# Kernel optimization log

Measured on AMD Instinct MI355X. Metric: run time of the kernel, lower is better.

## Reference

```python
import jax, jax.numpy as jnp
import numpy as np
from jax import lax

D = 768; H = 8; DQ = D // H; NL = 6; FF = 3072; MAXREL = 100; NOUT = 1024
B = 8; T = 4096; CIN = 8
EPS = 1e-5
NREL = 2 * MAXREL - 1  # 199 learned relative positions, rel in [-99, 99]


def conv1d(x, w, b, stride=1, pad=1):
    # x [B,C,T], w [O,I,K]
    y = lax.conv_general_dilated(x, w, (stride,), [(pad, pad)],
                                 dimension_numbers=('NCH', 'OIH', 'NCH'))
    return y + b[None, :, None]


def bnorm(x, p):
    # eval-mode BatchNorm1d; p [4,C] = (gamma, beta, running_mean, running_var)
    g, be, m, v = p[0], p[1], p[2], p[3]
    return g[None, :, None] * (x - m[None, :, None]) * lax.rsqrt(v[None, :, None] + EPS) + be[None, :, None]


def resblock(x, c1w, c1b, b1, c2w, c2b, b2, rw, rb, br):
    h = jax.nn.relu(bnorm(conv1d(x, c1w, c1b, stride=2), b1))
    h = bnorm(conv1d(h, c2w, c2b), b2)
    res = bnorm(conv1d(x, rw, rb, stride=2, pad=0), br)
    return jax.nn.relu(h + res)


def layer_norm(x, g, b):
    mu = jnp.mean(x, axis=-1, keepdims=True)
    var = jnp.mean(jnp.square(x - mu), axis=-1, keepdims=True)
    return g * (x - mu) * lax.rsqrt(var + EPS) + b


def attention(x, wq, wk, wv, wo, rel):
    # x [B,L,D]; wq/wk/wv [H,D,DQ]; wo [H,DQ,D]; rel [H,NREL,DQ]
    L = x.shape[1]
    q = jnp.einsum('bld,hdk->bhlk', x, wq)
    k = jnp.einsum('bld,hdk->bhlk', x, wk)
    v = jnp.einsum('bld,hdk->bhlk', x, wv)
    logits = jnp.einsum('bhqk,bhmk->bhqm', q, k) / np.float32(np.sqrt(DQ))
    # relative positional logits: pos[b,h,i,j] = q[b,h,i] . rel[h, (j-i)+99] if |j-i|<100 else -1e8
    rel_logits = jnp.einsum('bhlk,hmk->bhlm', q, rel)  # [B,H,L,NREL]
    pos_idx = jnp.arange(L)[None, :] - jnp.arange(L)[:, None] + (MAXREL - 1)  # j - i + 99
    valid = (pos_idx >= 0) & (pos_idx < NREL)
    idxc = jnp.clip(pos_idx, 0, NREL - 1)
    pos = jnp.take_along_axis(rel_logits, idxc[None, None, :, :], axis=3)  # [B,H,L,L]
    logits = logits + jnp.where(valid[None, None], pos, jnp.float32(-1e8))
    probs = jax.nn.softmax(logits, axis=-1)
    o = jnp.einsum('bhqm,bhmk->bhqk', probs, v)
    return jnp.einsum('bhlk,hkd->bld', o, wo)


def forward(x_raw, rb1_c1w, rb1_c1b, rb1_bn1, rb1_c2w, rb1_c2b, rb1_bn2, rb1_rw, rb1_rb, rb1_bnr,
            rb23_c1w, rb23_c1b, rb23_bn1, rb23_c2w, rb23_c2b, rb23_bn2, rb23_rw, rb23_rb, rb23_bnr,
            w_in_w, w_in_b, wq, wk, wv, wo, rel_emb, ln1_g, ln1_b, ln2_g, ln2_b,
            ff1_w, ff1_b, ff2_w, ff2_b, w_out_w, w_out_b):
    x = jnp.transpose(x_raw, (0, 2, 1))  # [B, 8, T]
    x = resblock(x, rb1_c1w, rb1_c1b, rb1_bn1, rb1_c2w, rb1_c2b, rb1_bn2, rb1_rw, rb1_rb, rb1_bnr)
    for i in range(2):
        x = resblock(x, rb23_c1w[i], rb23_c1b[i], rb23_bn1[i], rb23_c2w[i], rb23_c2b[i],
                     rb23_bn2[i], rb23_rw[i], rb23_rb[i], rb23_bnr[i])
    x = jnp.transpose(x, (0, 2, 1))  # [B, L=T/8, D]
    x = x @ w_in_w.T + w_in_b
    for l in range(NL):  # post-norm transformer encoder layers
        x = layer_norm(x + attention(x, wq[l], wk[l], wv[l], wo[l], rel_emb[l]), ln1_g[l], ln1_b[l])
        h = jax.nn.relu(x @ ff1_w[l].T + ff1_b[l]) @ ff2_w[l].T + ff2_b[l]
        x = layer_norm(x + h, ln2_g[l], ln2_b[l])
    return x @ w_out_w.T + w_out_b


def setup_inputs() -> dict:
    key = jax.random.key(0)
    ks = iter(jax.random.split(key, 128))

    def w(shape, scale):
        return jax.random.normal(next(ks), shape, dtype=jnp.float32) * scale

    def bnp(*lead):
        g = 1.0 + 0.1 * jax.random.normal(next(ks), (*lead, D), dtype=jnp.float32)
        be = 0.1 * jax.random.normal(next(ks), (*lead, D), dtype=jnp.float32)
        m = 0.1 * jax.random.normal(next(ks), (*lead, D), dtype=jnp.float32)
        v = jax.random.uniform(next(ks), (*lead, D), minval=0.5, maxval=1.5, dtype=jnp.float32)
        return jnp.stack([g, be, m, v], axis=-2)  # [..., 4, D]

    inp = {}
    inp['x_raw'] = jax.random.normal(next(ks), (B, T, CIN), dtype=jnp.float32)
    inp['rb1_c1w'] = w((D, CIN, 3), 0.2); inp['rb1_c1b'] = w((D,), 0.02); inp['rb1_bn1'] = bnp()
    inp['rb1_c2w'] = w((D, D, 3), 0.02); inp['rb1_c2b'] = w((D,), 0.02); inp['rb1_bn2'] = bnp()
    inp['rb1_rw'] = w((D, CIN, 1), 0.2); inp['rb1_rb'] = w((D,), 0.02); inp['rb1_bnr'] = bnp()
    inp['rb23_c1w'] = w((2, D, D, 3), 0.02); inp['rb23_c1b'] = w((2, D), 0.02); inp['rb23_bn1'] = bnp(2)
    inp['rb23_c2w'] = w((2, D, D, 3), 0.02); inp['rb23_c2b'] = w((2, D), 0.02); inp['rb23_bn2'] = bnp(2)
    inp['rb23_rw'] = w((2, D, D, 1), 0.02); inp['rb23_rb'] = w((2, D), 0.02); inp['rb23_bnr'] = bnp(2)
    inp['w_in_w'] = w((D, D), 0.02); inp['w_in_b'] = w((D,), 0.02)
    sd = D ** -0.5
    inp['wq'] = w((NL, H, D, DQ), sd); inp['wk'] = w((NL, H, D, DQ), sd)
    inp['wv'] = w((NL, H, D, DQ), sd); inp['wo'] = w((NL, H, DQ, D), sd)
    inp['rel_emb'] = w((NL, H, NREL, DQ), DQ ** -0.5)
    inp['ln1_g'] = jnp.ones((NL, D), jnp.float32); inp['ln1_b'] = jnp.zeros((NL, D), jnp.float32)
    inp['ln2_g'] = jnp.ones((NL, D), jnp.float32); inp['ln2_b'] = jnp.zeros((NL, D), jnp.float32)
    inp['ff1_w'] = w((NL, FF, D), 0.02); inp['ff1_b'] = w((NL, FF), 0.02)
    inp['ff2_w'] = w((NL, D, FF), 0.02); inp['ff2_b'] = w((NL, D), 0.02)
    inp['w_out_w'] = w((NOUT, D), 0.02); inp['w_out_b'] = w((NOUT,), 0.02)
    return inp


def reference(x_raw, rb1_c1w, rb1_c1b, rb1_bn1, rb1_c2w, rb1_c2b, rb1_bn2, rb1_rw, rb1_rb, rb1_bnr,
              rb23_c1w, rb23_c1b, rb23_bn1, rb23_c2w, rb23_c2b, rb23_bn2, rb23_rw, rb23_rb, rb23_bnr,
              w_in_w, w_in_b, wq, wk, wv, wo, rel_emb, ln1_g, ln1_b, ln2_g, ln2_b,
              ff1_w, ff1_b, ff2_w, ff2_b, w_out_w, w_out_b):
    return forward(x_raw, rb1_c1w, rb1_c1b, rb1_bn1, rb1_c2w, rb1_c2b, rb1_bn2, rb1_rw, rb1_rb, rb1_bnr,
                   rb23_c1w, rb23_c1b, rb23_bn1, rb23_c2w, rb23_c2b, rb23_bn2, rb23_rw, rb23_rb, rb23_bnr,
                   w_in_w, w_in_b, wq, wk, wv, wo, rel_emb, ln1_g, ln1_b, ln2_g, ln2_b,
                   ff1_w, ff1_b, ff2_w, ff2_b, w_out_w, w_out_b)
```

## Files before the change

kernel.cpp:

```cpp
#include <hip/hip_runtime.h>
#include <math.h>

typedef __bf16 bf16;
typedef bf16 bf16x8 __attribute__((ext_vector_type(8)));
typedef bf16 bf16x4 __attribute__((ext_vector_type(4)));
typedef float f32x4 __attribute__((ext_vector_type(4)));
#define EPSF 1e-5f

__device__ __forceinline__ void ldg_lds16(const bf16* g, bf16* l) {
    __builtin_amdgcn_global_load_lds((const __attribute__((address_space(1))) void*)g,
                                     (__attribute__((address_space(3))) void*)l, 16, 0, 0);
}

template<bool BIAS, bool RESF, bool RELU, bool WF, bool WB>
__global__ __launch_bounds__(256) void mgemm_k(
    const bf16* __restrict__ A, const bf16* __restrict__ B,
    const float* __restrict__ bias, const float* __restrict__ resf,
    float* __restrict__ Cf, bf16* __restrict__ Cb,
    int K, int lda, int ldb, int ldc, int Nstore,
    int Z2, long long sA1, long long sA2, long long sB1, long long sB2,
    long long sC1, long long sC2)
{
    int z = blockIdx.z;
    int z1 = z / Z2, z2 = z - z1 * Z2;
    A += z1 * sA1 + z2 * sA2;
    B += z1 * sB1 + z2 * sB2;
    long long coff = z1 * sC1 + z2 * sC2;

    __shared__ __align__(16) bf16 As[4096];
    __shared__ __align__(16) bf16 Bs[4096];
    int tid = threadIdx.x, wid = tid >> 6, lane = tid & 63;
    int m0 = blockIdx.y * 128, n0 = blockIdx.x * 128;
    int wr = wid >> 1, wc = wid & 1;
    int lrow = lane & 15, lk8 = (lane >> 4) * 8;
    int srow = wid * 32 + (lane >> 2);
    int scol = (lane & 3) * 8;
    f32x4 acc[4][4] = {};

    for (int kt = 0; kt < K; kt += 32) {
        ldg_lds16(A + (size_t)(m0 + srow) * lda + kt + scol, As + wid * 1024);
        ldg_lds16(A + (size_t)(m0 + srow + 16) * lda + kt + scol, As + wid * 1024 + 512);
        ldg_lds16(B + (size_t)(n0 + srow) * ldb + kt + scol, Bs + wid * 1024);
        ldg_lds16(B + (size_t)(n0 + srow + 16) * ldb + kt + scol, Bs + wid * 1024 + 512);
        __syncthreads();
        bf16x8 af[4], bfr[4];
#pragma unroll
        for (int i = 0; i < 4; i++) {
            af[i]  = *(const bf16x8*)(As + (wr * 64 + i * 16 + lrow) * 32 + lk8);
            bfr[i] = *(const bf16x8*)(Bs + (wc * 64 + i * 16 + lrow) * 32 + lk8);
        }
#pragma unroll
        for (int i = 0; i < 4; i++)
#pragma unroll
            for (int j = 0; j < 4; j++)
                acc[i][j] = __builtin_amdgcn_mfma_f32_16x16x32_bf16(af[i], bfr[j], acc[i][j], 0, 0, 0);
        __syncthreads();
    }
    int mtop = m0 + wr * 64 + (lane >> 4) * 4;
    int ntop = n0 + wc * 64 + lrow;
#pragma unroll
    for (int mi = 0; mi < 4; mi++) {
#pragma unroll
        for (int r = 0; r < 4; r++) {
            int m = mtop + mi * 16 + r;
            long long ro = coff + (long long)m * ldc;
#pragma unroll
            for (int ni = 0; ni < 4; ni++) {
                int n = ntop + ni * 16;
                float v = acc[mi][ni][r];
                if (BIAS) v += bias[n];
                if (RESF) v += resf[ro + n];
                if (RELU) v = fmaxf(v, 0.f);
                if (n < Nstore) {
                    if (WF) Cf[ro + n] = v;
                    if (WB) Cb[ro + n] = (bf16)v;
                }
            }
        }
    }
}

template<bool RES, bool RELU>
__global__ __launch_bounds__(256) void conv_k(
    const bf16* __restrict__ in, const bf16* __restrict__ w,
    const float* __restrict__ scsh, const bf16* __restrict__ res, bf16* __restrict__ out,
    int KK, int stride, int rowoff, long long instrideB, long long outstrideB, int outoff,
    long long resstrideB)
{
    int z = blockIdx.z;
    int n0 = blockIdx.x * 128, m0 = blockIdx.y * 128;
    __shared__ __align__(16) bf16 As[4096];
    __shared__ __align__(16) bf16 Bs[4096];
    int tid = threadIdx.x, wid = tid >> 6, lane = tid & 63;
    int wr = wid >> 1, wc = wid & 1;
    int lrow = lane & 15, lk8 = (lane >> 4) * 8;
    int srow = wid * 32 + (lane >> 2);
    int scol = (lane & 3) * 8;
    const bf16* inz = in + (size_t)z * instrideB;
    f32x4 acc[4][4] = {};

    for (int kt = 0; kt < KK; kt += 32) {
        int kq = kt / 768;
        int ic0 = kt - kq * 768;
        ldg_lds16(inz + (size_t)((m0 + srow) * stride + kq + rowoff) * 768 + ic0 + scol, As + wid * 1024);
        ldg_lds16(inz + (size_t)((m0 + srow + 16) * stride + kq + rowoff) * 768 + ic0 + scol, As + wid * 1024 + 512);
        ldg_lds16(w + (size_t)(n0 + srow) * KK + kt + scol, Bs + wid * 1024);
        ldg_lds16(w + (size_t)(n0 + srow + 16) * KK + kt + scol, Bs + wid * 1024 + 512);
        __syncthreads();
        bf16x8 af[4], bfr[4];
#pragma unroll
        for (int i = 0; i < 4; i++) {
            af[i]  = *(const bf16x8*)(As + (wr * 64 + i * 16 + lrow) * 32 + lk8);
            bfr[i] = *(const bf16x8*)(Bs + (wc * 64 + i * 16 + lrow) * 32 + lk8);
        }
#pragma unroll
        for (int i = 0; i < 4; i++)
#pragma unroll
            for (int j = 0; j < 4; j++)
                acc[i][j] = __builtin_amdgcn_mfma_f32_16x16x32_bf16(af[i], bfr[j], acc[i][j], 0, 0, 0);
        __syncthreads();
    }
    bf16* outz = out + (size_t)z * outstrideB + (size_t)outoff * 768;
    const bf16* resz = res + (RES ? (size_t)z * resstrideB : 0);
    int mtop = m0 + wr * 64 + (lane >> 4) * 4;
    int ntop = n0 + wc * 64 + lrow;
#pragma unroll
    for (int mi = 0; mi < 4; mi++) {
#pragma unroll
        for (int r = 0; r < 4; r++) {
            int m = mtop + mi * 16 + r;
#pragma unroll
            for (int ni = 0; ni < 4; ni++) {
                int n = ntop + ni * 16;
                float v = acc[mi][ni][r] * scsh[n] + scsh[768 + n];
                if (RES) v += (float)resz[(size_t)m * 768 + n];
                if (RELU) v = fmaxf(v, 0.f);
                outz[(size_t)m * 768 + n] = (bf16)v;
            }
        }
    }
}

__global__ __launch_bounds__(256) void qkrel_k(
    const bf16* __restrict__ qkv, const float* __restrict__ relb, float* __restrict__ lg)
{
    int z = blockIdx.z, b = z >> 3, h = z & 7;
    int i0 = blockIdx.y * 128, j0 = blockIdx.x * 128;
    long long lgbase = (long long)z * 262144;
    int tid = threadIdx.x;
    if (i0 - j0 > 226 || j0 - i0 > 226) {
        float4 f = make_float4(-1e8f, -1e8f, -1e8f, -1e8f);
        int rr0 = tid >> 4, cc = (tid & 15) * 8;
#pragma unroll
        for (int s = 0; s < 8; s++) {
            float* p = lg + lgbase + (long long)(i0 + s * 16 + rr0) * 512 + j0 + cc;
            ((float4*)p)[0] = f; ((float4*)p)[1] = f;
        }
        return;
    }
    const bf16* Aq = qkv + (size_t)b * 512 * 2304 + h * 96;
    const bf16* Bk = Aq + 768;
    __shared__ __align__(16) bf16 As[4096];
    __shared__ __align__(16) bf16 Bs[4096];
    int wid = tid >> 6, lane = tid & 63;
    int wr = wid >> 1, wc = wid & 1;
    int lrow = lane & 15, lk8 = (lane >> 4) * 8;
    int srow = wid * 32 + (lane >> 2);
    int scol = (lane & 3) * 8;
    f32x4 acc[4][4] = {};
    for (int kt = 0; kt < 96; kt += 32) {
        ldg_lds16(Aq + (size_t)(i0 + srow) * 2304 + kt + scol, As + wid * 1024);
        ldg_lds16(Aq + (size_t)(i0 + srow + 16) * 2304 + kt + scol, As + wid * 1024 + 512);
        ldg_lds16(Bk + (size_t)(j0 + srow) * 2304 + kt + scol, Bs + wid * 1024);
        ldg_lds16(Bk + (size_t)(j0 + srow + 16) * 2304 + kt + scol, Bs + wid * 1024 + 512);
        __syncthreads();
        bf16x8 af[4], bfr[4];
#pragma unroll
        for (int i = 0; i < 4; i++) {
            af[i]  = *(const bf16x8*)(As + (wr * 64 + i * 16 + lrow) * 32 + lk8);
            bfr[i] = *(const bf16x8*)(Bs + (wc * 64 + i * 16 + lrow) * 32 + lk8);
        }
#pragma unroll
        for (int i = 0; i < 4; i++)
#pragma unroll
            for (int j = 0; j < 4; j++)
                acc[i][j] = __builtin_amdgcn_mfma_f32_16x16x32_bf16(af[i], bfr[j], acc[i][j], 0, 0, 0);
        __syncthreads();
    }
    const float sc = 0.10206207261596577f;
    int itop = i0 + wr * 64 + (lane >> 4) * 4;
    int jtop = j0 + wc * 64 + lrow;
#pragma unroll
    for (int mi = 0; mi < 4; mi++) {
#pragma unroll
        for (int r = 0; r < 4; r++) {
            int i = itop + mi * 16 + r;
            const float* rrow = relb + ((long long)h * 4096 + b * 512 + i) * 256;
#pragma unroll
            for (int ni = 0; ni < 4; ni++) {
                int j = jtop + ni * 16;
                float v = acc[mi][ni][r] * sc;
                int idx = j - i + 99;
                v += (idx >= 0 && idx < 199) ? rrow[idx] : -1e8f;
                lg[lgbase + (long long)i * 512 + j] = v;
            }
        }
    }
}

__global__ __launch_bounds__(256) void softmax_k(float* __restrict__ lg)
{
    __shared__ float red1[4];
    __shared__ float red2[4];
    size_t r = blockIdx.x;
    float* p = lg + r * 512;
    int tid = threadIdx.x;
    float v0 = p[tid], v1 = p[tid + 256];
    float m = fmaxf(v0, v1);
#pragma unroll
    for (int off = 32; off; off >>= 1) m = fmaxf(m, __shfl_xor(m, off));
    if ((tid & 63) == 0) red1[tid >> 6] = m;
    __syncthreads();
    m = fmaxf(fmaxf(red1[0], red1[1]), fmaxf(red1[2], red1[3]));
    float e0 = expf(v0 - m), e1 = expf(v1 - m);
    float s = e0 + e1;
#pragma unroll
    for (int off = 32; off; off >>= 1) s += __shfl_xor(s, off);
    if ((tid & 63) == 0) red2[tid >> 6] = s;
    __syncthreads();
    float inv = 1.f / (red2[0] + red2[1] + red2[2] + red2[3]);
    bf16* pb = (bf16*)p;
    pb[tid] = (bf16)(e0 * inv);
    pb[tid + 256] = (bf16)(e1 * inv);
}

__global__ __launch_bounds__(256) void ln2_k(const float* __restrict__ in,
                                             const float* __restrict__ g,
                                             const float* __restrict__ b,
                                             float* __restrict__ xf, bf16* __restrict__ xb)
{
    __shared__ float red1[4];
    __shared__ float red2[4];
    int r = blockIdx.x, tid = threadIdx.x;
    const float* p = in + (size_t)r * 768;
    float x0 = p[tid], x1 = p[tid + 256], x2 = p[tid + 512];
    float s = x0 + x1 + x2;
#pragma unroll
    for (int off = 32; off; off >>= 1) s += __shfl_xor(s, off);
    if ((tid & 63) == 0) red1[tid >> 6] = s;
    __syncthreads();
    float mu = (red1[0] + red1[1] + red1[2] + red1[3]) * (1.f / 768.f);
    float d0 = x0 - mu, d1 = x1 - mu, d2 = x2 - mu;
    float sq = d0 * d0 + d1 * d1 + d2 * d2;
#pragma unroll
    for (int off = 32; off; off >>= 1) sq += __shfl_xor(sq, off);
    if ((tid & 63) == 0) red2[tid >> 6] = sq;
    __syncthreads();
    float rstd = rsqrtf((red2[0] + red2[1] + red2[2] + red2[3]) * (1.f / 768.f) + EPSF);
    float o0 = g[tid] * d0 * rstd + b[tid];
    float o1 = g[tid + 256] * d1 * rstd + b[tid + 256];
    float o2 = g[tid + 512] * d2 * rstd + b[tid + 512];
    size_t base = (size_t)r * 768;
    xf[base + tid] = o0;       xb[base + tid] = (bf16)o0;
    xf[base + tid + 256] = o1; xb[base + tid + 256] = (bf16)o1;
    xf[base + tid + 512] = o2; xb[base + tid + 512] = (bf16)o2;
}

__global__ __launch_bounds__(256) void rb1_front_k(
    const float* __restrict__ xr, const float* __restrict__ c1w, const float* __restrict__ rw,
    const float* __restrict__ scsh0, const float* __restrict__ scsh1,
    bf16* __restrict__ h1, bf16* __restrict__ res1)
{
    int t = blockIdx.x, b = blockIdx.y, tid = threadIdx.x;
    const float* xb = xr + (size_t)b * 4096 * 8;
    float xv[3][8];
#pragma unroll
    for (int k = 0; k < 3; k++) {
        int pos = 2 * t + k - 1;
        bool ok = (unsigned)pos < 4096u;
        const float* xp = xb + (size_t)pos * 8;
#pragma unroll
        for (int c = 0; c < 8; c++) xv[k][c] = ok ? xp[c] : 0.f;
    }
#pragma unroll
    for (int rep = 0; rep < 3; rep++) {
        int o = rep * 256 + tid;
        float conv = 0.f;
        const float* wp = c1w + (size_t)o * 24;
#pragma unroll
        for (int c = 0; c < 8; c++)
#pragma unroll
            for (int k = 0; k < 3; k++) conv = fmaf(wp[c * 3 + k], xv[k][c], conv);
        float hv = fmaxf(conv * scsh0[o] + scsh0[768 + o], 0.f);
        h1[((size_t)b * 2050 + t + 1) * 768 + o] = (bf16)hv;
        float cr = 0.f;
        const float* rp = rw + (size_t)o * 8;
#pragma unroll
        for (int c = 0; c < 8; c++) cr = fmaf(rp[c], xv[1][c], cr);
        res1[((size_t)b * 2048 + t) * 768 + o] = (bf16)(cr * scsh1[o] + scsh1[768 + o]);
    }
}

__global__ void bnprep_k(const float* __restrict__ bn, const float* __restrict__ cb,
                         float* __restrict__ scsh)
{
    int i = blockIdx.x * 256 + threadIdx.x;
    if (i >= 768) return;
    float g = bn[i], be = bn[768 + i], m = bn[1536 + i], v = bn[2304 + i];
    float sc = g * rsqrtf(v + EPSF);
    scsh[i] = sc;
    scsh[768 + i] = (cb[i] - m) * sc + be;
}

__global__ void zeropad_k(bf16* __restrict__ buf, int T)
{
    int i = blockIdx.x * 256 + threadIdx.x;
    if (i >= 768) return;
    int row = blockIdx.y ? (T + 1) : 0;
    buf[((size_t)blockIdx.z * (T + 2) + row) * 768 + i] = (bf16)0.f;
}

__global__ void rep3_k(const float* __restrict__ w, bf16* __restrict__ wr)
{
    long long i = (long long)blockIdx.x * 256 + threadIdx.x;
    if (i >= 1769472) return;
    int o = i / 2304, k = i - (long long)o * 2304;
    int kq = k / 768, ic = k - kq * 768;
    wr[i] = (bf16)w[((long long)o * 768 + ic) * 3 + kq];
}

__global__ void cast4_k(const float* __restrict__ s, bf16* __restrict__ d, int n4)
{
    int i = blockIdx.x * 256 + threadIdx.x;
    if (i >= n4) return;
    float4 v = ((const float4*)s)[i];
    bf16x4 o = {(bf16)v.x, (bf16)v.y, (bf16)v.z, (bf16)v.w};
    ((bf16x4*)d)[i] = o;
}

__global__ void layerprep_k(const float* __restrict__ wq, const float* __restrict__ wk,
                            const float* __restrict__ wv, const float* __restrict__ wo,
                            const float* __restrict__ rel,
                            const float* __restrict__ ff1, const float* __restrict__ ff2,
                            bf16* __restrict__ Wqkv, bf16* __restrict__ Wo,
                            bf16* __restrict__ Rel, bf16* __restrict__ F1, bf16* __restrict__ F2)
{
    long long i = (long long)blockIdx.x * 256 + threadIdx.x;
    const long long S0 = 1769472, S1 = 589824, S2 = 196608, S3 = 2359296;
    if (i < S0) {
        int n = i / 768, k = i - (long long)n * 768;
        int sel = n / 768, hq = n - sel * 768;
        int h = hq / 96, q = hq - h * 96;
        const float* src = sel == 0 ? wq : (sel == 1 ? wk : wv);
        Wqkv[i] = (bf16)src[((long long)h * 768 + k) * 96 + q];
    } else if (i < S0 + S1) {
        long long j = i - S0;
        int n = j / 768, kk = j - (long long)n * 768;
        Wo[j] = (bf16)wo[(long long)kk * 768 + n];
    } else if (i < S0 + S1 + S2) {
        long long j = i - S0 - S1;
        int h = j / 24576, rest = j - (long long)h * 24576;
        int rr = rest / 96, q = rest - rr * 96;
        Rel[j] = rr < 199 ? (bf16)rel[((long long)h * 199 + rr) * 96 + q] : (bf16)0.f;
    } else if (i < S0 + S1 + S2 + S3) {
        long long j = i - S0 - S1 - S2;
        F1[j] = (bf16)ff1[j];
    } else {
        long long j = i - S0 - S1 - S2 - S3;
        F2[j] = (bf16)ff2[j];
    }
}

__global__ __launch_bounds__(256) void vt_k(const bf16* __restrict__ qkv, bf16* __restrict__ vt)
{
    int z = blockIdx.z, b = z >> 3, h = z & 7;
    int t0 = blockIdx.x * 32, q0 = blockIdx.y * 32;
    __shared__ bf16 sm[32][33];
    int tx = threadIdx.x & 31, ty = threadIdx.x >> 5;
#pragma unroll
    for (int s = 0; s < 4; s++) {
        int t = t0 + ty + s * 8, q = q0 + tx;
        sm[ty + s * 8][tx] = (q < 96) ? qkv[((size_t)b * 512 + t) * 2304 + 1536 + h * 96 + q]
                                      : (bf16)0.f;
    }
    __syncthreads();
#pragma unroll
    for (int s = 0; s < 4; s++) {
        int q = q0 + ty + s * 8;
        vt[((size_t)z * 128 + q) * 512 + t0 + tx] = sm[tx][ty + s * 8];
    }
}

extern "C" void kernel_launch(void* const* d_in, const int* in_sizes, int n_in,
                              void* d_out, int out_size, void* d_ws, size_t ws_size,
                              hipStream_t stream)
{
    const float* x_raw    = (const float*)d_in[0];
    const float* rb1_c1w  = (const float*)d_in[1];
    const float* rb1_c1b  = (const float*)d_in[2];
    const float* rb1_bn1  = (const float*)d_in[3];
    const float* rb1_c2w  = (const float*)d_in[4];
    const float* rb1_c2b  = (const float*)d_in[5];
    const float* rb1_bn2  = (const float*)d_in[6];
    const float* rb1_rw   = (const float*)d_in[7];
    const float* rb1_rb   = (const float*)d_in[8];
    const float* rb1_bnr  = (const float*)d_in[9];
    const float* rb23_c1w = (const float*)d_in[10];
    const float* rb23_c1b = (const float*)d_in[11];
    const float* rb23_bn1 = (const float*)d_in[12];
    const float* rb23_c2w = (const float*)d_in[13];
    const float* rb23_c2b = (const float*)d_in[14];
    const float* rb23_bn2 = (const float*)d_in[15];
    const float* rb23_rw  = (const float*)d_in[16];
    const float* rb23_rb  = (const float*)d_in[17];
    const float* rb23_bnr = (const float*)d_in[18];
    const float* w_in_w   = (const float*)d_in[19];
    const float* w_in_b   = (const float*)d_in[20];
    const float* wq       = (const float*)d_in[21];
    const float* wk       = (const float*)d_in[22];
    const float* wv       = (const float*)d_in[23];
    const float* wo       = (const float*)d_in[24];
    const float* rel_emb  = (const float*)d_in[25];
    const float* ln1_g    = (const float*)d_in[26];
    const float* ln1_b    = (const float*)d_in[27];
    const float* ln2_g    = (const float*)d_in[28];
    const float* ln2_b    = (const float*)d_in[29];
    const float* ff1_w    = (const float*)d_in[30];
    const float* ff1_b    = (const float*)d_in[31];
    const float* ff2_w    = (const float*)d_in[32];
    const float* ff2_b    = (const float*)d_in[33];
    const float* w_out_w  = (const float*)d_in[34];
    const float* w_out_b  = (const float*)d_in[35];
    float* out = (float*)d_out;

    char* W = (char*)d_ws;
    bf16*  h1buf  = (bf16*)(W + 0);
    bf16*  resbuf = (bf16*)(W + 26000000);
    bf16*  xbuf   = (bf16*)(W + 52000000);
    float* lg     = (float*)(W + 0);
    bf16*  wc3    = (bf16*)(W + 78000000);
    bf16*  wc1    = (bf16*)(W + 82000000);
    float* scsh   = (float*)(W + 84000000);
    float* xf     = (float*)(W + 85000000);
    bf16*  xb     = (bf16*)(W + 98000000);
    bf16*  qkv    = (bf16*)(W + 105000000);
    bf16*  vt     = (bf16*)(W + 124000000);
    float* relb   = (float*)(W + 133000000);
    bf16*  ffh    = (bf16*)(W + 133000000);
    bf16*  atno   = (bf16*)(W + 167000000);
    float* tmp    = (float*)(W + 174000000);
    bf16*  Wqkv   = (bf16*)(W + 187000000);
    bf16*  Wo     = (bf16*)(W + 191000000);
    bf16*  F1     = (bf16*)(W + 193000000);
    bf16*  F2     = (bf16*)(W + 198000000);
    bf16*  Relp   = (bf16*)(W + 203000000);
    bf16*  Wout   = (bf16*)(W + 204000000);
    bf16*  Winw   = (bf16*)(W + 206000000);

    bnprep_k<<<3, 256, 0, stream>>>(rb1_bn1, rb1_c1b, scsh + 0 * 1536);
    bnprep_k<<<3, 256, 0, stream>>>(rb1_bnr, rb1_rb,  scsh + 1 * 1536);
    bnprep_k<<<3, 256, 0, stream>>>(rb1_bn2, rb1_c2b, scsh + 2 * 1536);
    bnprep_k<<<3, 256, 0, stream>>>(rb23_bn1, rb23_c1b, scsh + 3 * 1536);
    bnprep_k<<<3, 256, 0, stream>>>(rb23_bnr, rb23_rb,  scsh + 4 * 1536);
    bnprep_k<<<3, 256, 0, stream>>>(rb23_bn2, rb23_c2b, scsh + 5 * 1536);
    bnprep_k<<<3, 256, 0, stream>>>(rb23_bn1 + 3072, rb23_c1b + 768, scsh + 6 * 1536);
    bnprep_k<<<3, 256, 0, stream>>>(rb23_bnr + 3072, rb23_rb + 768,  scsh + 7 * 1536);
    bnprep_k<<<3, 256, 0, stream>>>(rb23_bn2 + 3072, rb23_c2b + 768, scsh + 8 * 1536);

    rb1_front_k<<<dim3(2048, 8), 256, 0, stream>>>(x_raw, rb1_c1w, rb1_rw,
                                                   scsh, scsh + 1536, h1buf, resbuf);
    zeropad_k<<<dim3(3, 2, 8), 256, 0, stream>>>(h1buf, 2048);
    rep3_k<<<6912, 256, 0, stream>>>(rb1_c2w, wc3);
    conv_k<true, true><<<dim3(6, 16, 8), 256, 0, stream>>>(
        h1buf, wc3, scsh + 2 * 1536, resbuf, xbuf, 2304, 1, 0,
        (long long)2050 * 768, (long long)2050 * 768, 1, (long long)2048 * 768);
    zeropad_k<<<dim3(3, 2, 8), 256, 0, stream>>>(xbuf, 2048);
    rep3_k<<<6912, 256, 0, stream>>>(rb23_c1w, wc3);
    conv_k<false, true><<<dim3(6, 8, 8), 256, 0, stream>>>(
        xbuf, wc3, scsh + 3 * 1536, nullptr, h1buf, 2304, 2, 0,
        (long long)2050 * 768, (long long)1026 * 768, 1, 0);
    zeropad_k<<<dim3(3, 2, 8), 256, 0, stream>>>(h1buf, 1024);
    cast4_k<<<576, 256, 0, stream>>>(rb23_rw, wc1, 147456);
    conv_k<false, false><<<dim3(6, 8, 8), 256, 0, stream>>>(
        xbuf, wc1, scsh + 4 * 1536, nullptr, resbuf, 768, 2, 1,
        (long long)2050 * 768, (long long)1024 * 768, 0, 0);
    rep3_k<<<6912, 256, 0, stream>>>(rb23_c2w, wc3);
    conv_k<true, true><<<dim3(6, 8, 8), 256, 0, stream>>>(
        h1buf, wc3, scsh + 5 * 1536, resbuf, xbuf, 2304, 1, 0,
        (long long)1026 * 768, (long long)1026 * 768, 1, (long long)1024 * 768);
    zeropad_k<<<dim3(3, 2, 8), 256, 0, stream>>>(xbuf, 1024);
    rep3_k<<<6912, 256, 0, stream>>>(rb23_c1w + 1769472, wc3);
    conv_k<false, true><<<dim3(6, 4, 8), 256, 0, stream>>>(
        xbuf, wc3, scsh + 6 * 1536, nullptr, h1buf, 2304, 2, 0,
        (long long)1026 * 768, (long long)514 * 768, 1, 0);
    zeropad_k<<<dim3(3, 2, 8), 256, 0, stream>>>(h1buf, 512);
    cast4_k<<<576, 256, 0, stream>>>(rb23_rw + 589824, wc1, 147456);
    conv_k<false, false><<<dim3(6, 4, 8), 256, 0, stream>>>(
        xbuf, wc1, scsh + 7 * 1536, nullptr, resbuf, 768, 2, 1,
        (long long)1026 * 768, (long long)512 * 768, 0, 0);
    rep3_k<<<6912, 256, 0, stream>>>(rb23_c2w + 1769472, wc3);
    conv_k<true, true><<<dim3(6, 4, 8), 256, 0, stream>>>(
        h1buf, wc3, scsh + 8 * 1536, resbuf, xbuf, 2304, 1, 0,
        (long long)514 * 768, (long long)512 * 768, 0, (long long)512 * 768);

    cast4_k<<<576, 256, 0, stream>>>(w_in_w, Winw, 147456);
    cast4_k<<<768, 256, 0, stream>>>(w_out_w, Wout, 196608);
    mgemm_k<true, false, false, true, true><<<dim3(6, 32, 1), 256, 0, stream>>>(
        xbuf, Winw, w_in_b, nullptr, xf, xb, 768, 768, 768, 768, 768, 1, 0, 0, 0, 0, 0, 0);

    for (int l = 0; l < 6; l++) {
        layerprep_k<<<28416, 256, 0, stream>>>(
            wq + (size_t)l * 589824, wk + (size_t)l * 589824, wv + (size_t)l * 589824,
            wo + (size_t)l * 589824, rel_emb + (size_t)l * 152832,
            ff1_w + (size_t)l * 2359296, ff2_w + (size_t)l * 2359296,
            Wqkv, Wo, Relp, F1, F2);
        mgemm_k<false, false, false, false, true><<<dim3(18, 32, 1), 256, 0, stream>>>(
            xb, Wqkv, nullptr, nullptr, nullptr, qkv, 768, 768, 768, 2304, 2304,
            1, 0, 0, 0, 0, 0, 0);
        vt_k<<<dim3(16, 4, 64), 256, 0, stream>>>(qkv, vt);
        mgemm_k<false, false, false, true, false><<<dim3(2, 32, 8), 256, 0, stream>>>(
            qkv, Relp, nullptr, nullptr, relb, nullptr, 96, 2304, 96, 256, 256,
            1, 96, 0, 24576, 0, 1048576, 0);
        qkrel_k<<<dim3(4, 4, 64), 256, 0, stream>>>(qkv, relb, lg);
        softmax_k<<<32768, 256, 0, stream>>>(lg);
        mgemm_k<false, false, false, false, true><<<dim3(1, 4, 64), 256, 0, stream>>>(
            (const bf16*)lg, vt, nullptr, nullptr, nullptr, atno, 512, 1024, 512, 768, 96,
            8, 4194304, 524288, 524288, 65536, 393216, 96);
        mgemm_k<false, true, false, true, false><<<dim3(6, 32, 1), 256, 0, stream>>>(
            atno, Wo, nullptr, xf, tmp, nullptr, 768, 768, 768, 768, 768,
            1, 0, 0, 0, 0, 0, 0);
        ln2_k<<<4096, 256, 0, stream>>>(tmp, ln1_g + l * 768, ln1_b + l * 768, xf, xb);
        mgemm_k<true, false, true, false, true><<<dim3(24, 32, 1), 256, 0, stream>>>(
            xb, F1, ff1_b + l * 3072, nullptr, nullptr, ffh, 768, 768, 768, 3072, 3072,
            1, 0, 0, 0, 0, 0, 0);
        mgemm_k<true, true, false, true, false><<<dim3(6, 32, 1), 256, 0, stream>>>(
            ffh, F2, ff2_b + l * 768, xf, tmp, nullptr, 3072, 3072, 3072, 768, 768,
            1, 0, 0, 0, 0, 0, 0);
        ln2_k<<<4096, 256, 0, stream>>>(tmp, ln2_g + l * 768, ln2_b + l * 768, xf, xb);
    }

    mgemm_k<true, false, false, true, false><<<dim3(8, 32, 1), 256, 0, stream>>>(
        xb, Wout, w_out_b, nullptr, out, nullptr, 768, 768, 768, 1024, 1024,
        1, 0, 0, 0, 0, 0, 0);
}
```

Measured before the change: 3.079 ms.

## Double-buffer GEMM/conv loads, swizzle for XCDs, and skip out-of-band attention tiles

```diff
diff --git a/kernel.cpp b/kernel.cpp
--- a/kernel.cpp
+++ b/kernel.cpp
@@ -12,7 +12,13 @@
                                      (__attribute__((address_space(3))) void*)l, 16, 0, 0);
 }
 
-template<bool BIAS, bool RESF, bool RELU, bool WF, bool WB>
+__device__ __forceinline__ int xcd_swz(int orig, int nwg) {
+    int xcd = orig & 7, base = orig >> 3;
+    int q = nwg >> 3, r = nwg & 7;
+    return (xcd < r ? xcd * (q + 1) : r * (q + 1) + (xcd - r) * q) + base;
+}
+
+template<bool BIAS, bool RESF, bool RELU, bool WF, bool WB, bool BAND>
 __global__ __launch_bounds__(256) void mgemm_k(
     const bf16* __restrict__ A, const bf16* __restrict__ B,
     const float* __restrict__ bias, const float* __restrict__ resf,
@@ -27,27 +33,51 @@
     B += z1 * sB1 + z2 * sB2;
     long long coff = z1 * sC1 + z2 * sC2;
 
-    __shared__ __align__(16) bf16 As[4096];
-    __shared__ __align__(16) bf16 Bs[4096];
+    int bx = blockIdx.x, by = blockIdx.y;
+    int nwg = gridDim.x * gridDim.y;
+    if ((nwg & 7) == 0 && nwg >= 16) {
+        int id = xcd_swz(by * gridDim.x + bx, nwg);
+        bx = id % gridDim.x; by = id / gridDim.x;
+    }
+
+    __shared__ __align__(16) bf16 As[8192];
+    __shared__ __align__(16) bf16 Bs[8192];
     int tid = threadIdx.x, wid = tid >> 6, lane = tid & 63;
-    int m0 = blockIdx.y * 128, n0 = blockIdx.x * 128;
+    int m0 = by * 128, n0 = bx * 128;
     int wr = wid >> 1, wc = wid & 1;
     int lrow = lane & 15, lk8 = (lane >> 4) * 8;
     int srow = wid * 32 + (lane >> 2);
     int scol = (lane & 3) * 8;
     f32x4 acc[4][4] = {};
 
-    for (int kt = 0; kt < K; kt += 32) {
-        ldg_lds16(A + (size_t)(m0 + srow) * lda + kt + scol, As + wid * 1024);
-        ldg_lds16(A + (size_t)(m0 + srow + 16) * lda + kt + scol, As + wid * 1024 + 512);
-        ldg_lds16(B + (size_t)(n0 + srow) * ldb + kt + scol, Bs + wid * 1024);
-        ldg_lds16(B + (size_t)(n0 + srow + 16) * ldb + kt + scol, Bs + wid * 1024 + 512);
-        __syncthreads();
+    int ktlo = 0, nt;
+    if (BAND) {
+        int lo = m0 - 99; if (lo < 0) lo = 0;
+        ktlo = (lo >> 5) << 5;
+        int hi = ((m0 + 226) >> 5) * 32 + 32;
+        if (hi > K) hi = K;
+        nt = (hi - ktlo) >> 5;
+    } else {
+        nt = K >> 5;
+    }
+
+#define STAGE_AB(cur, kt) do { \
+    ldg_lds16(A + (size_t)(m0 + srow) * lda + (kt) + scol, As + (cur) * 4096 + wid * 1024); \
+    ldg_lds16(A + (size_t)(m0 + srow + 16) * lda + (kt) + scol, As + (cur) * 4096 + wid * 1024 + 512); \
+    ldg_lds16(B + (size_t)(n0 + srow) * ldb + (kt) + scol, Bs + (cur) * 4096 + wid * 1024); \
+    ldg_lds16(B + (size_t)(n0 + srow + 16) * ldb + (kt) + scol, Bs + (cur) * 4096 + wid * 1024 + 512); \
+} while (0)
+
+    STAGE_AB(0, ktlo);
+    __syncthreads();
+    for (int t = 0; t < nt; t++) {
+        int cur = t & 1;
+        if (t + 1 < nt) STAGE_AB(cur ^ 1, ktlo + (t + 1) * 32);
         bf16x8 af[4], bfr[4];
 #pragma unroll
         for (int i = 0; i < 4; i++) {
-            af[i]  = *(const bf16x8*)(As + (wr * 64 + i * 16 + lrow) * 32 + lk8);
-            bfr[i] = *(const bf16x8*)(Bs + (wc * 64 + i * 16 + lrow) * 32 + lk8);
+            af[i]  = *(const bf16x8*)(As + cur * 4096 + (wr * 64 + i * 16 + lrow) * 32 + lk8);
+            bfr[i] = *(const bf16x8*)(Bs + cur * 4096 + (wc * 64 + i * 16 + lrow) * 32 + lk8);
         }
 #pragma unroll
         for (int i = 0; i < 4; i++)
@@ -56,6 +86,8 @@
                 acc[i][j] = __builtin_amdgcn_mfma_f32_16x16x32_bf16(af[i], bfr[j], acc[i][j], 0, 0, 0);
         __syncthreads();
     }
+#undef STAGE_AB
+
     int mtop = m0 + wr * 64 + (lane >> 4) * 4;
     int ntop = n0 + wc * 64 + lrow;
 #pragma unroll
@@ -88,9 +120,15 @@
     long long resstrideB)
 {
     int z = blockIdx.z;
-    int n0 = blockIdx.x * 128, m0 = blockIdx.y * 128;
-    __shared__ __align__(16) bf16 As[4096];
-    __shared__ __align__(16) bf16 Bs[4096];
+    int bx = blockIdx.x, by = blockIdx.y;
+    int nwg = gridDim.x * gridDim.y;
+    if ((nwg & 7) == 0 && nwg >= 16) {
+        int id = xcd_swz(by * gridDim.x + bx, nwg);
+        bx = id % gridDim.x; by = id / gridDim.x;
+    }
+    int n0 = bx * 128, m0 = by * 128;
+    __shared__ __align__(16) bf16 As[8192];
+    __shared__ __align__(16) bf16 Bs[8192];
     int tid = threadIdx.x, wid = tid >> 6, lane = tid & 63;
     int wr = wid >> 1, wc = wid & 1;
     int lrow = lane & 15, lk8 = (lane >> 4) * 8;
@@ -98,20 +136,27 @@
     int scol = (lane & 3) * 8;
     const bf16* inz = in + (size_t)z * instrideB;
     f32x4 acc[4][4] = {};
-
-    for (int kt = 0; kt < KK; kt += 32) {
-        int kq = kt / 768;
-        int ic0 = kt - kq * 768;
-        ldg_lds16(inz + (size_t)((m0 + srow) * stride + kq + rowoff) * 768 + ic0 + scol, As + wid * 1024);
-        ldg_lds16(inz + (size_t)((m0 + srow + 16) * stride + kq + rowoff) * 768 + ic0 + scol, As + wid * 1024 + 512);
-        ldg_lds16(w + (size_t)(n0 + srow) * KK + kt + scol, Bs + wid * 1024);
-        ldg_lds16(w + (size_t)(n0 + srow + 16) * KK + kt + scol, Bs + wid * 1024 + 512);
-        __syncthreads();
+    int nt = KK >> 5;
+
+#define STAGE_CV(cur, kt) do { \
+    int kq_ = (kt) / 768; \
+    int ic0_ = (kt) - kq_ * 768; \
+    ldg_lds16(inz + (size_t)((m0 + srow) * stride + kq_ + rowoff) * 768 + ic0_ + scol, As + (cur) * 4096 + wid * 1024); \
+    ldg_lds16(inz + (size_t)((m0 + srow + 16) * stride + kq_ + rowoff) * 768 + ic0_ + scol, As + (cur) * 4096 + wid * 1024 + 512); \
+    ldg_lds16(w + (size_t)(n0 + srow) * KK + (kt) + scol, Bs + (cur) * 4096 + wid * 1024); \
+    ldg_lds16(w + (size_t)(n0 + srow + 16) * KK + (kt) + scol, Bs + (cur) * 4096 + wid * 1024 + 512); \
+} while (0)
+
+    STAGE_CV(0, 0);
+    __syncthreads();
+    for (int t = 0; t < nt; t++) {
+        int cur = t & 1;
+        if (t + 1 < nt) STAGE_CV(cur ^ 1, (t + 1) * 32);
         bf16x8 af[4], bfr[4];
 #pragma unroll
         for (int i = 0; i < 4; i++) {
-            af[i]  = *(const bf16x8*)(As + (wr * 64 + i * 16 + lrow) * 32 + lk8);
-            bfr[i] = *(const bf16x8*)(Bs + (wc * 64 + i * 16 + lrow) * 32 + lk8);
+            af[i]  = *(const bf16x8*)(As + cur * 4096 + (wr * 64 + i * 16 + lrow) * 32 + lk8);
+            bfr[i] = *(const bf16x8*)(Bs + cur * 4096 + (wc * 64 + i * 16 + lrow) * 32 + lk8);
         }
 #pragma unroll
         for (int i = 0; i < 4; i++)
@@ -120,6 +165,8 @@
                 acc[i][j] = __builtin_amdgcn_mfma_f32_16x16x32_bf16(af[i], bfr[j], acc[i][j], 0, 0, 0);
         __syncthreads();
     }
+#undef STAGE_CV
+
     bf16* outz = out + (size_t)z * outstrideB + (size_t)outoff * 768;
     const bf16* resz = res + (RES ? (size_t)z * resstrideB : 0);
     int mtop = m0 + wr * 64 + (lane >> 4) * 4;
@@ -141,44 +188,43 @@
     }
 }
 
+__device__ const int qk_ti[10] = {0, 0, 1, 1, 1, 2, 2, 2, 3, 3};
+__device__ const int qk_tj[10] = {0, 1, 0, 1, 2, 1, 2, 3, 2, 3};
+
 __global__ __launch_bounds__(256) void qkrel_k(
     const bf16* __restrict__ qkv, const float* __restrict__ relb, float* __restrict__ lg)
 {
     int z = blockIdx.z, b = z >> 3, h = z & 7;
-    int i0 = blockIdx.y * 128, j0 = blockIdx.x * 128;
+    int i0 = qk_ti[blockIdx.x] * 128, j0 = qk_tj[blockIdx.x] * 128;
     long long lgbase = (long long)z * 262144;
-    int tid = threadIdx.x;
-    if (i0 - j0 > 226 || j0 - i0 > 226) {
-        float4 f = make_float4(-1e8f, -1e8f, -1e8f, -1e8f);
-        int rr0 = tid >> 4, cc = (tid & 15) * 8;
-#pragma unroll
-        for (int s = 0; s < 8; s++) {
-            float* p = lg + lgbase + (long long)(i0 + s * 16 + rr0) * 512 + j0 + cc;
-            ((float4*)p)[0] = f; ((float4*)p)[1] = f;
-        }
-        return;
-    }
     const bf16* Aq = qkv + (size_t)b * 512 * 2304 + h * 96;
     const bf16* Bk = Aq + 768;
-    __shared__ __align__(16) bf16 As[4096];
-    __shared__ __align__(16) bf16 Bs[4096];
-    int wid = tid >> 6, lane = tid & 63;
+    __shared__ __align__(16) bf16 As[8192];
+    __shared__ __align__(16) bf16 Bs[8192];
+    int tid = threadIdx.x, wid = tid >> 6, lane = tid & 63;
     int wr = wid >> 1, wc = wid & 1;
     int lrow = lane & 15, lk8 = (lane >> 4) * 8;
     int srow = wid * 32 + (lane >> 2);
     int scol = (lane & 3) * 8;
     f32x4 acc[4][4] = {};
-    for (int kt = 0; kt < 96; kt += 32) {
-        ldg_lds16(Aq + (size_t)(i0 + srow) * 2304 + kt + scol, As + wid * 1024);
-        ldg_lds16(Aq + (size_t)(i0 + srow + 16) * 2304 + kt + scol, As + wid * 1024 + 512);
-        ldg_lds16(Bk + (size_t)(j0 + srow) * 2304 + kt + scol, Bs + wid * 1024);
-        ldg_lds16(Bk + (size_t)(j0 + srow + 16) * 2304 + kt + scol, Bs + wid * 1024 + 512);
-        __syncthreads();
+
+#define STAGE_QK(cur, kt) do { \
+    ldg_lds16(Aq + (size_t)(i0 + srow) * 2304 + (kt) + scol, As + (cur) * 4096 + wid * 1024); \
+    ldg_lds16(Aq + (size_t)(i0 + srow + 16) * 2304 + (kt) + scol, As + (cur) * 4096 + wid * 1024 + 512); \
+    ldg_lds16(Bk + (size_t)(j0 + srow) * 2304 + (kt) + scol, Bs + (cur) * 4096 + wid * 1024); \
+    ldg_lds16(Bk + (size_t)(j0 + srow + 16) * 2304 + (kt) + scol, Bs + (cur) * 4096 + wid * 1024 + 512); \
+} while (0)
+
+    STAGE_QK(0, 0);
+    __syncthreads();
+    for (int t = 0; t < 3; t++) {
+        int cur = t & 1;
+        if (t + 1 < 3) STAGE_QK(cur ^ 1, (t + 1) * 32);
         bf16x8 af[4], bfr[4];
 #pragma unroll
         for (int i = 0; i < 4; i++) {
-            af[i]  = *(const bf16x8*)(As + (wr * 64 + i * 16 + lrow) * 32 + lk8);
-            bfr[i] = *(const bf16x8*)(Bs + (wc * 64 + i * 16 + lrow) * 32 + lk8);
+            af[i]  = *(const bf16x8*)(As + cur * 4096 + (wr * 64 + i * 16 + lrow) * 32 + lk8);
+            bfr[i] = *(const bf16x8*)(Bs + cur * 4096 + (wc * 64 + i * 16 + lrow) * 32 + lk8);
         }
 #pragma unroll
         for (int i = 0; i < 4; i++)
@@ -187,6 +233,8 @@
                 acc[i][j] = __builtin_amdgcn_mfma_f32_16x16x32_bf16(af[i], bfr[j], acc[i][j], 0, 0, 0);
         __syncthreads();
     }
+#undef STAGE_QK
+
     const float sc = 0.10206207261596577f;
     int itop = i0 + wr * 64 + (lane >> 4) * 4;
     int jtop = j0 + wc * 64 + lrow;
@@ -213,25 +261,32 @@
     __shared__ float red1[4];
     __shared__ float red2[4];
     size_t r = blockIdx.x;
+    int i = (int)(r & 511);
+    int jlo = i - 99; if (jlo < 0) jlo = 0;
+    int jhi = i + 100; if (jhi > 512) jhi = 512;
     float* p = lg + r * 512;
     int tid = threadIdx.x;
-    float v0 = p[tid], v1 = p[tid + 256];
-    float m = fmaxf(v0, v1);
+    int j = jlo + tid;
+    bool act = j < jhi;
+    float v = act ? p[j] : -1e30f;
+    float m = v;
 #pragma unroll
     for (int off = 32; off; off >>= 1) m = fmaxf(m, __shfl_xor(m, off));
     if ((tid & 63) == 0) red1[tid >> 6] = m;
     __syncthreads();
     m = fmaxf(fmaxf(red1[0], red1[1]), fmaxf(red1[2], red1[3]));
-    float e0 = expf(v0 - m), e1 = expf(v1 - m);
-    float s = e0 + e1;
+    float e = act ? expf(v - m) : 0.f;
+    float s = e;
 #pragma unroll
     for (int off = 32; off; off >>= 1) s += __shfl_xor(s, off);
     if ((tid & 63) == 0) red2[tid >> 6] = s;
     __syncthreads();
     float inv = 1.f / (red2[0] + red2[1] + red2[2] + red2[3]);
     bf16* pb = (bf16*)p;
-    pb[tid] = (bf16)(e0 * inv);
-    pb[tid + 256] = (bf16)(e1 * inv);
+    if (act) pb[j] = (bf16)(e * inv);
+#pragma unroll
+    for (int c = tid; c < 512; c += 256)
+        if (c < jlo || c >= jhi) pb[c] = (bf16)0.f;
 }
 
 __global__ __launch_bounds__(256) void ln2_k(const float* __restrict__ in,
@@ -505,7 +560,7 @@
 
     cast4_k<<<576, 256, 0, stream>>>(w_in_w, Winw, 147456);
     cast4_k<<<768, 256, 0, stream>>>(w_out_w, Wout, 196608);
-    mgemm_k<true, false, false, true, true><<<dim3(6, 32, 1), 256, 0, stream>>>(
+    mgemm_k<true, false, false, true, true, false><<<dim3(6, 32, 1), 256, 0, stream>>>(
         xbuf, Winw, w_in_b, nullptr, xf, xb, 768, 768, 768, 768, 768, 1, 0, 0, 0, 0, 0, 0);
 
     for (int l = 0; l < 6; l++) {
@@ -514,32 +569,32 @@
             wo + (size_t)l * 589824, rel_emb + (size_t)l * 152832,
             ff1_w + (size_t)l * 2359296, ff2_w + (size_t)l * 2359296,
             Wqkv, Wo, Relp, F1, F2);
-        mgemm_k<false, false, false, false, true><<<dim3(18, 32, 1), 256, 0, stream>>>(
+        mgemm_k<false, false, false, false, true, false><<<dim3(18, 32, 1), 256, 0, stream>>>(
             xb, Wqkv, nullptr, nullptr, nullptr, qkv, 768, 768, 768, 2304, 2304,
             1, 0, 0, 0, 0, 0, 0);
         vt_k<<<dim3(16, 4, 64), 256, 0, stream>>>(qkv, vt);
-        mgemm_k<false, false, false, true, false><<<dim3(2, 32, 8), 256, 0, stream>>>(
+        mgemm_k<false, false, false, true, false, false><<<dim3(2, 32, 8), 256, 0, stream>>>(
             qkv, Relp, nullptr, nullptr, relb, nullptr, 96, 2304, 96, 256, 256,
             1, 96, 0, 24576, 0, 1048576, 0);
-        qkrel_k<<<dim3(4, 4, 64), 256, 0, stream>>>(qkv, relb, lg);
+        qkrel_k<<<dim3(10, 1, 64), 256, 0, stream>>>(qkv, relb, lg);
         softmax_k<<<32768, 256, 0, stream>>>(lg);
-        mgemm_k<false, false, false, false, true><<<dim3(1, 4, 64), 256, 0, stream>>>(
+        mgemm_k<false, false, false, false, true, true><<<dim3(1, 4, 64), 256, 0, stream>>>(
             (const bf16*)lg, vt, nullptr, nullptr, nullptr, atno, 512, 1024, 512, 768, 96,
             8, 4194304, 524288, 524288, 65536, 393216, 96);
-        mgemm_k<false, true, false, true, false><<<dim3(6, 32, 1), 256, 0, stream>>>(
+        mgemm_k<false, true, false, true, false, false><<<dim3(6, 32, 1), 256, 0, stream>>>(
             atno, Wo, nullptr, xf, tmp, nullptr, 768, 768, 768, 768, 768,
             1, 0, 0, 0, 0, 0, 0);
         ln2_k<<<4096, 256, 0, stream>>>(tmp, ln1_g + l * 768, ln1_b + l * 768, xf, xb);
-        mgemm_k<true, false, true, false, true><<<dim3(24, 32, 1), 256, 0, stream>>>(
+        mgemm_k<true, false, true, false, true, false><<<dim3(24, 32, 1), 256, 0, stream>>>(
             xb, F1, ff1_b + l * 3072, nullptr, nullptr, ffh, 768, 768, 768, 3072, 3072,
             1, 0, 0, 0, 0, 0, 0);
-        mgemm_k<true, true, false, true, false><<<dim3(6, 32, 1), 256, 0, stream>>>(
+        mgemm_k<true, true, false, true, false, false><<<dim3(6, 32, 1), 256, 0, stream>>>(
             ffh, F2, ff2_b + l * 768, xf, tmp, nullptr, 3072, 3072, 3072, 768, 768,
             1, 0, 0, 0, 0, 0, 0);
         ln2_k<<<4096, 256, 0, stream>>>(tmp, ln2_g + l * 768, ln2_b + l * 768, xf, xb);
     }
 
-    mgemm_k<true, false, false, true, false><<<dim3(8, 32, 1), 256, 0, stream>>>(
+    mgemm_k<true, false, false, true, false, false><<<dim3(8, 32, 1), 256, 0, stream>>>(
         xb, Wout, w_out_b, nullptr, out, nullptr, 768, 768, 768, 1024, 1024,
         1, 0, 0, 0, 0, 0, 0);
 }
```

After: 2.591 ms. -15.8%, faster.
